# Performance work log

Hardware: AMD Instinct MI355X
Metric: run time of the kernel (lower is better)

The kernel has to match this reference:

```python
import jax, jax.numpy as jnp
import numpy as np

NUM_NODES = 100000
EMBED_DIM = 64
NUM_EDGES = 1200000
NUM_LAYERS = 3
ALPHA = 0.25  # 1 / (num_layers + 1)


def setup_inputs() -> dict:
    key = jax.random.key(0)
    k1, k2, k3, k4 = jax.random.split(key, 4)
    x = jax.random.normal(k1, (NUM_NODES, EMBED_DIM), dtype=jnp.float32)
    edge_attr = jax.random.uniform(k2, (NUM_EDGES,), dtype=jnp.float32)
    edge_index = jax.random.randint(k3, (2, NUM_EDGES), 0, NUM_NODES, dtype=jnp.int64)
    edge_mask = jax.random.randint(k4, (NUM_EDGES,), 0, 2, dtype=jnp.int32).astype(jnp.bool_)
    return {"x": x, "edge_attr": edge_attr, "edge_index": edge_index, "edge_mask": edge_mask}


def reference(x, edge_attr, edge_index, edge_mask):
    # Masked edge selection == zeroing masked edge weights (same degree & aggregation).
    w = edge_attr * edge_mask.astype(edge_attr.dtype)  # [E]
    row, col = edge_index[0], edge_index[1]            # source, target

    # gcn_norm with add_self_loops=False: D^{-1/2} A D^{-1/2}
    deg = jax.ops.segment_sum(w, col, num_segments=NUM_NODES)          # [N]
    dinv = jnp.where(deg > 0, jax.lax.rsqrt(deg), 0.0)                 # [N]
    norm = dinv[row] * w * dinv[col]                                   # [E]

    out = ALPHA * x
    h = x
    for _ in range(NUM_LAYERS):
        msg = norm[:, None] * h[row]                                   # [E, D] gather
        h = jax.ops.segment_sum(msg, col, num_segments=NUM_NODES)      # [N, D] scatter
        out = out + ALPHA * h
    return out
```

## Files before the change

### kernel.cpp

```cpp
#include <hip/hip_runtime.h>
#include <hip/hip_fp16.h>

#define N_NODES 100000
#define EMB     64
#define N_EDGES 1200000
#define CAP     32
#define ALPHA   0.25f

__global__ void k_detect(const unsigned char* __restrict__ maskB,
                         const int* __restrict__ idx, int* __restrict__ flags,
                         int* __restrict__ cnt) {
    int tid = blockIdx.x * blockDim.x + threadIdx.x;
    int lane = threadIdx.x & 63;
    bool mev = (tid & 3) && maskB[tid];
    if (__any(mev) && lane == 0) atomicOr(&flags[0], 1);
    bool iev = (tid < 4096) && (idx[2 * tid + 1] != 0);
    if (__any(iev) && lane == 0) atomicOr(&flags[1], 1);
    for (int i = tid; i < N_NODES; i += 64 * 256) cnt[i] = 0;
}

__device__ __forceinline__ int idx_row(const int* idx, int i64, int e) {
    return i64 ? idx[2 * e] : idx[e];
}
__device__ __forceinline__ int idx_col(const int* idx, int i64, int e) {
    return i64 ? idx[2 * (N_EDGES + e)] : idx[N_EDGES + e];
}
__device__ __forceinline__ int edge_mask(const void* maskp, int mbool, int e) {
    return mbool ? (int)((const unsigned char*)maskp)[e] : ((const int*)maskp)[e];
}

__global__ void k_histfill(const float* __restrict__ ea, const void* maskp,
                           const int* __restrict__ idx,
                           const int* __restrict__ flags,
                           int* __restrict__ cnt, int2* __restrict__ staged) {
    int e = blockIdx.x * blockDim.x + threadIdx.x;
    if (e >= N_EDGES) return;
    int mbool = flags[0] != 0, i64 = (flags[1] == 0);
    if (!edge_mask(maskp, mbool, e)) return;
    float wv = ea[e];
    if (wv == 0.0f) return;
    int c = idx_col(idx, i64, e);
    if ((unsigned)c >= N_NODES) return;
    int r = idx_row(idx, i64, e);
    int rok = (unsigned)r < N_NODES;
    int rank = atomicAdd(&cnt[c], 1);
    if (rank < CAP)
        staged[c * CAP + rank] = make_int2(__float_as_int(rok ? wv : 0.0f),
                                           rok ? r : 0);
}

__global__ __launch_bounds__(256) void k_degconv(
        const int* __restrict__ cnt, int2* __restrict__ staged,
        const float4* __restrict__ x4, float4* __restrict__ t0,
        float* __restrict__ dinv, float* __restrict__ sd) {
    int t = blockIdx.x * blockDim.x + threadIdx.x;
    int n = t >> 3;
    int q = t & 7;
    if (n >= N_NODES) return;
    int c = cnt[n];
    if (c < 0) c = 0;
    if (c > CAP) c = CAP;
    int2* base = staged + n * CAP;
    float s = 0.0f;
    for (int j = q; j < c; j += 8) s += __int_as_float(base[j].x);
    s += __shfl_xor(s, 1);
    s += __shfl_xor(s, 2);
    s += __shfl_xor(s, 4);
    int pc = (c + 3) & ~3;
    if (q < pc - c) base[c + q] = make_int2(0, 0);
    float di = (s > 0.0f) ? rsqrtf(s) : 0.0f;
    if (q == 0) {
        dinv[n] = di;
        sd[n] = (s > 0.0f) ? sqrtf(s) : 0.0f;
    }
    size_t xb = (size_t)n * 16 + q * 2;
    float4 v0 = x4[xb], v1 = x4[xb + 1];
    float4 o;
    __half2* op = reinterpret_cast<__half2*>(&o);
    op[0] = __floats2half2_rn(di * v0.x, di * v0.y);
    op[1] = __floats2half2_rn(di * v0.z, di * v0.w);
    op[2] = __floats2half2_rn(di * v1.x, di * v1.y);
    op[3] = __floats2half2_rn(di * v1.z, di * v1.w);
    t0[(size_t)n * 8 + q] = o;
}

__device__ __forceinline__ void accum_h8(float4& sa, float4& sb, float w,
                                         float4 raw) {
    const __half2* hp = reinterpret_cast<const __half2*>(&raw);
    float2 f0 = __half22float2(hp[0]);
    float2 f1 = __half22float2(hp[1]);
    float2 f2 = __half22float2(hp[2]);
    float2 f3 = __half22float2(hp[3]);
    sa.x += w * f0.x; sa.y += w * f0.y; sa.z += w * f1.x; sa.w += w * f1.y;
    sb.x += w * f2.x; sb.y += w * f2.y; sb.z += w * f3.x; sb.w += w * f3.y;
}

__device__ __forceinline__ void gather_core_f16(
        const int2* __restrict__ base, int c, const float4* __restrict__ h16,
        int q, float4& sa, float4& sb) {
    sa = make_float4(0.f, 0.f, 0.f, 0.f);
    sb = make_float4(0.f, 0.f, 0.f, 0.f);
    if (c <= 0) return;
    int nb = ((c + 3) & ~3) >> 2;
    const int4* csr4 = (const int4*)base;
    for (int t = 0; t < nb; ++t) {
        int4 pa = csr4[2 * t];
        int4 pb = csr4[2 * t + 1];
        float w0 = __int_as_float(pa.x);
        float w1 = __int_as_float(pa.z);
        float w2 = __int_as_float(pb.x);
        float w3 = __int_as_float(pb.z);
        int r0 = min((unsigned)pa.y, (unsigned)(N_NODES - 1));
        int r1 = min((unsigned)pa.w, (unsigned)(N_NODES - 1));
        int r2 = min((unsigned)pb.y, (unsigned)(N_NODES - 1));
        int r3 = min((unsigned)pb.w, (unsigned)(N_NODES - 1));
        float4 v0 = h16[(size_t)r0 * 8 + q];
        float4 v1 = h16[(size_t)r1 * 8 + q];
        float4 v2 = h16[(size_t)r2 * 8 + q];
        float4 v3 = h16[(size_t)r3 * 8 + q];
        accum_h8(sa, sb, w0, v0);
        accum_h8(sa, sb, w1, v1);
        accum_h8(sa, sb, w2, v2);
        accum_h8(sa, sb, w3, v3);
    }
}

__global__ __launch_bounds__(256) void k_gather_mid(
        const int* __restrict__ cnt, const int2* __restrict__ staged,
        const float* __restrict__ dinv,
        const float4* __restrict__ tsrc, float4* __restrict__ tdst) {
    int t = blockIdx.x * blockDim.x + threadIdx.x;
    int n = t >> 3;
    int q = t & 7;
    if (n >= N_NODES) return;
    int c = cnt[n];
    if (c > CAP) c = CAP;
    const int2* base = staged + n * CAP;
    float4 sa, sb;
    gather_core_f16(base, c, tsrc, q, sa, sb);
    float di = dinv[n];
    float d2 = di * di;
    float4 o;
    __half2* op = reinterpret_cast<__half2*>(&o);
    op[0] = __floats2half2_rn(d2 * sa.x, d2 * sa.y);
    op[1] = __floats2half2_rn(d2 * sa.z, d2 * sa.w);
    op[2] = __floats2half2_rn(d2 * sb.x, d2 * sb.y);
    op[3] = __floats2half2_rn(d2 * sb.z, d2 * sb.w);
    tdst[(size_t)n * 8 + q] = o;
}

__global__ __launch_bounds__(256) void k_gather_last(
        const int* __restrict__ cnt, const int2* __restrict__ staged,
        const float* __restrict__ dinv, const float* __restrict__ sd,
        const float4* __restrict__ x4, const float4* __restrict__ t1_16,
        const float4* __restrict__ t2_16, float4* __restrict__ out4) {
    int t = blockIdx.x * blockDim.x + threadIdx.x;
    int n = t >> 3;
    int q = t & 7;
    if (n >= N_NODES) return;
    int c = cnt[n];
    if (c > CAP) c = CAP;
    const int2* base = staged + n * CAP;
    float4 sa, sb;
    gather_core_f16(base, c, t2_16, q, sa, sb);
    float di = dinv[n];
    float sdv = sd[n];
    size_t o8 = (size_t)n * 8 + q;
    float4 r1 = t1_16[o8];
    float4 r2 = t2_16[o8];
    const __half2* a1 = reinterpret_cast<const __half2*>(&r1);
    const __half2* a2 = reinterpret_cast<const __half2*>(&r2);
    float2 b10 = __half22float2(a1[0]), b11 = __half22float2(a1[1]);
    float2 b12 = __half22float2(a1[2]), b13 = __half22float2(a1[3]);
    float2 b20 = __half22float2(a2[0]), b21 = __half22float2(a2[1]);
    float2 b22 = __half22float2(a2[2]), b23 = __half22float2(a2[3]);
    size_t ox = (size_t)n * 16 + 2 * q;
    float4 x0 = x4[ox], x1 = x4[ox + 1];
    float4 o0, o1;
    o0.x = ALPHA * (x0.x + sdv * (b10.x + b20.x) + di * sa.x);
    o0.y = ALPHA * (x0.y + sdv * (b10.y + b20.y) + di * sa.y);
    o0.z = ALPHA * (x0.z + sdv * (b11.x + b21.x) + di * sa.z);
    o0.w = ALPHA * (x0.w + sdv * (b11.y + b21.y) + di * sa.w);
    o1.x = ALPHA * (x1.x + sdv * (b12.x + b22.x) + di * sb.x);
    o1.y = ALPHA * (x1.y + sdv * (b12.y + b22.y) + di * sb.y);
    o1.z = ALPHA * (x1.z + sdv * (b13.x + b23.x) + di * sb.z);
    o1.w = ALPHA * (x1.w + sdv * (b13.y + b23.y) + di * sb.w);
    out4[ox] = o0;
    out4[ox + 1] = o1;
}

extern "C" void kernel_launch(void* const* d_in, const int* in_sizes, int n_in,
                              void* d_out, int out_size, void* d_ws, size_t ws_size,
                              hipStream_t stream) {
    const float* x   = (const float*)d_in[0];
    const float* ea  = (const float*)d_in[1];
    const int*   idx = (const int*)d_in[2];
    const void*  msk = d_in[3];
    float*       out = (float*)d_out;

    char* ws = (char*)d_ws;
    size_t off = 0;
    auto alloc = [&](size_t bytes) -> void* {
        void* p = ws + off;
        off = (off + bytes + 255) & ~(size_t)255;
        return p;
    };
    int*    flags  = (int*)   alloc(64);
    int*    cnt    = (int*)   alloc(sizeof(int)  * N_NODES);
    float*  dinv   = (float*) alloc(sizeof(float) * N_NODES);
    float*  sd     = (float*) alloc(sizeof(float) * N_NODES);
    int2*   staged = (int2*)  alloc(sizeof(int2) * (size_t)N_NODES * CAP);
    float4* t0     = (float4*)alloc(sizeof(unsigned short) * (size_t)N_NODES * EMB);
    float4* tA     = (float4*)alloc(sizeof(unsigned short) * (size_t)N_NODES * EMB);
    float4* tB     = (float4*)alloc(sizeof(unsigned short) * (size_t)N_NODES * EMB);

    const int B = 256;
    const int gE = (N_EDGES + B - 1) / B;
    const int gG = (N_NODES * 8 + B - 1) / B;

    (void)hipMemsetAsync(flags, 0, 64, stream);
    k_detect  <<<64, 256, 0, stream>>>((const unsigned char*)msk, idx, flags, cnt);
    k_histfill<<<gE, B, 0, stream>>>(ea, msk, idx, flags, cnt, staged);
    k_degconv <<<gG, B, 0, stream>>>(cnt, staged, (const float4*)x, t0, dinv, sd);

    k_gather_mid <<<gG, B, 0, stream>>>(cnt, staged, dinv, t0, tA);
    k_gather_mid <<<gG, B, 0, stream>>>(cnt, staged, dinv, tA, tB);
    k_gather_last<<<gG, B, 0, stream>>>(cnt, staged, dinv, sd,
                                        (const float4*)x, tA, tB, (float4*)out);
}
```

Before: 187.2 us.

## Fuse degree-norm and propagation layers into one cooperative persistent kernel

Merges the degree/convert kernel and the three gather layers into a single cooperative kernel launched with a fixed grid of 1536 blocks. The blocks loop over nodes with a grid stride and use grid-wide syncs between stages. The aim is to remove the launch gaps and tail effects of four separate launches. In exchange it adds grid-sync costs and relies on occupancy of 6 blocks per CU. It falls back to the separate launches if the cooperative launch fails.

```diff
diff --git a/kernel.cpp b/kernel.cpp
--- a/kernel.cpp
+++ b/kernel.cpp
@@ -1,11 +1,15 @@
 #include <hip/hip_runtime.h>
 #include <hip/hip_fp16.h>
+#include <hip/hip_cooperative_groups.h>
+
+namespace cg = cooperative_groups;
 
 #define N_NODES 100000
 #define EMB     64
 #define N_EDGES 1200000
 #define CAP     32
 #define ALPHA   0.25f
+#define GRID_COOP 1536
 
 __global__ void k_detect(const unsigned char* __restrict__ maskB,
                          const int* __restrict__ idx, int* __restrict__ flags,
@@ -49,14 +53,13 @@
                                            rok ? r : 0);
 }
 
-__global__ __launch_bounds__(256) void k_degconv(
-        const int* __restrict__ cnt, int2* __restrict__ staged,
+
+__device__ __forceinline__ void degconv_body(
+        int t, const int* __restrict__ cnt, int2* __restrict__ staged,
         const float4* __restrict__ x4, float4* __restrict__ t0,
         float* __restrict__ dinv, float* __restrict__ sd) {
-    int t = blockIdx.x * blockDim.x + threadIdx.x;
     int n = t >> 3;
     int q = t & 7;
-    if (n >= N_NODES) return;
     int c = cnt[n];
     if (c < 0) c = 0;
     if (c > CAP) c = CAP;
@@ -125,14 +128,12 @@
     }
 }
 
-__global__ __launch_bounds__(256) void k_gather_mid(
-        const int* __restrict__ cnt, const int2* __restrict__ staged,
+__device__ __forceinline__ void gather_mid_body(
+        int t, const int* __restrict__ cnt, const int2* __restrict__ staged,
         const float* __restrict__ dinv,
         const float4* __restrict__ tsrc, float4* __restrict__ tdst) {
-    int t = blockIdx.x * blockDim.x + threadIdx.x;
     int n = t >> 3;
     int q = t & 7;
-    if (n >= N_NODES) return;
     int c = cnt[n];
     if (c > CAP) c = CAP;
     const int2* base = staged + n * CAP;
@@ -149,15 +150,13 @@
     tdst[(size_t)n * 8 + q] = o;
 }
 
-__global__ __launch_bounds__(256) void k_gather_last(
-        const int* __restrict__ cnt, const int2* __restrict__ staged,
+__device__ __forceinline__ void gather_last_body(
+        int t, const int* __restrict__ cnt, const int2* __restrict__ staged,
         const float* __restrict__ dinv, const float* __restrict__ sd,
         const float4* __restrict__ x4, const float4* __restrict__ t1_16,
         const float4* __restrict__ t2_16, float4* __restrict__ out4) {
-    int t = blockIdx.x * blockDim.x + threadIdx.x;
     int n = t >> 3;
     int q = t & 7;
-    if (n >= N_NODES) return;
     int c = cnt[n];
     if (c > CAP) c = CAP;
     const int2* base = staged + n * CAP;
@@ -189,6 +188,54 @@
     out4[ox + 1] = o1;
 }
 
+__global__ __launch_bounds__(256, 6) void k_fused(
+        const int* __restrict__ cnt, int2* __restrict__ staged,
+        const float4* __restrict__ x4, float4* __restrict__ t0,
+        float4* __restrict__ tA, float4* __restrict__ tB,
+        float4* __restrict__ out4, float* __restrict__ dinv,
+        float* __restrict__ sd) {
+    cg::grid_group grid = cg::this_grid();
+    const int base = blockIdx.x * blockDim.x + threadIdx.x;
+    const int stride = GRID_COOP * 256;
+    for (int t = base; t < N_NODES * 8; t += stride)
+        degconv_body(t, cnt, staged, x4, t0, dinv, sd);
+    grid.sync();
+    for (int t = base; t < N_NODES * 8; t += stride)
+        gather_mid_body(t, cnt, staged, dinv, t0, tA);
+    grid.sync();
+    for (int t = base; t < N_NODES * 8; t += stride)
+        gather_mid_body(t, cnt, staged, dinv, tA, tB);
+    grid.sync();
+    for (int t = base; t < N_NODES * 8; t += stride)
+        gather_last_body(t, cnt, staged, dinv, sd, x4, tA, tB, out4);
+}
+
+__global__ __launch_bounds__(256) void k_degconv(
+        const int* __restrict__ cnt, int2* __restrict__ staged,
+        const float4* __restrict__ x4, float4* __restrict__ t0,
+        float* __restrict__ dinv, float* __restrict__ sd) {
+    int t = blockIdx.x * blockDim.x + threadIdx.x;
+    if (t >= N_NODES * 8) return;
+    degconv_body(t, cnt, staged, x4, t0, dinv, sd);
+}
+__global__ __launch_bounds__(256) void k_gather_mid(
+        const int* __restrict__ cnt, const int2* __restrict__ staged,
+        const float* __restrict__ dinv,
+        const float4* __restrict__ tsrc, float4* __restrict__ tdst) {
+    int t = blockIdx.x * blockDim.x + threadIdx.x;
+    if (t >= N_NODES * 8) return;
+    gather_mid_body(t, cnt, staged, dinv, tsrc, tdst);
+}
+__global__ __launch_bounds__(256) void k_gather_last(
+        const int* __restrict__ cnt, const int2* __restrict__ staged,
+        const float* __restrict__ dinv, const float* __restrict__ sd,
+        const float4* __restrict__ x4, const float4* __restrict__ t1_16,
+        const float4* __restrict__ t2_16, float4* __restrict__ out4) {
+    int t = blockIdx.x * blockDim.x + threadIdx.x;
+    if (t >= N_NODES * 8) return;
+    gather_last_body(t, cnt, staged, dinv, sd, x4, t1_16, t2_16, out4);
+}
+
 extern "C" void kernel_launch(void* const* d_in, const int* in_sizes, int n_in,
                               void* d_out, int out_size, void* d_ws, size_t ws_size,
                               hipStream_t stream) {
@@ -221,10 +268,20 @@
     (void)hipMemsetAsync(flags, 0, 64, stream);
     k_detect  <<<64, 256, 0, stream>>>((const unsigned char*)msk, idx, flags, cnt);
     k_histfill<<<gE, B, 0, stream>>>(ea, msk, idx, flags, cnt, staged);
-    k_degconv <<<gG, B, 0, stream>>>(cnt, staged, (const float4*)x, t0, dinv, sd);
-
-    k_gather_mid <<<gG, B, 0, stream>>>(cnt, staged, dinv, t0, tA);
-    k_gather_mid <<<gG, B, 0, stream>>>(cnt, staged, dinv, tA, tB);
-    k_gather_last<<<gG, B, 0, stream>>>(cnt, staged, dinv, sd,
-                                        (const float4*)x, tA, tB, (float4*)out);
-}
+
+    const float4* x4p  = (const float4*)x;
+    float4*       outp = (float4*)out;
+    void* args[] = {(void*)&cnt, (void*)&staged, (void*)&x4p, (void*)&t0,
+                    (void*)&tA, (void*)&tB, (void*)&outp, (void*)&dinv,
+                    (void*)&sd};
+    hipError_t cerr = hipLaunchCooperativeKernel((const void*)k_fused,
+                                                 dim3(GRID_COOP), dim3(B),
+                                                 args, 0, stream);
+    if (cerr != hipSuccess) {
+        k_degconv    <<<gG, B, 0, stream>>>(cnt, staged, x4p, t0, dinv, sd);
+        k_gather_mid <<<gG, B, 0, stream>>>(cnt, staged, dinv, t0, tA);
+        k_gather_mid <<<gG, B, 0, stream>>>(cnt, staged, dinv, tA, tB);
+        k_gather_last<<<gG, B, 0, stream>>>(cnt, staged, dinv, sd,
+                                            x4p, tA, tB, outp);
+    }
+}
```

After: 656.0 us. 250% more time.
